# Optimization experiments

Hardware: AMD Instinct MI355X
Metric: run time of the kernel (lower is better)

The kernel has to match this reference:

```python
import jax, jax.numpy as jnp
import numpy as np

V, D, H, F, L, B, S = 32000, 1024, 16, 4096, 6, 2, 1024
DH = D // H


def setup_inputs() -> dict:
    key = jax.random.key(0)
    ks = jax.random.split(key, 12)
    n = lambda k, shape: jax.random.normal(k, shape, jnp.float32) * 0.02
    inp = {}
    inp['x'] = jax.random.randint(ks[0], (B, S), 0, V)
    # causal mask: 1 = masked (upper triangle), matches masked_fill(mask==1, -inf)
    inp['mask'] = jnp.triu(jnp.ones((S, S), jnp.int32), k=1)[None, None]
    inp['embed'] = n(ks[1], (V, D))
    inp['wq'] = n(ks[2], (L, D, D)); inp['bq'] = jnp.zeros((L, D), jnp.float32)
    inp['wk'] = n(ks[3], (L, D, D)); inp['bk'] = jnp.zeros((L, D), jnp.float32)
    inp['wv'] = n(ks[4], (L, D, D)); inp['bv'] = jnp.zeros((L, D), jnp.float32)
    inp['wo'] = n(ks[5], (L, D, D)); inp['bo'] = jnp.zeros((L, D), jnp.float32)
    inp['w1'] = n(ks[6], (L, D, F)); inp['b1'] = jnp.zeros((L, F), jnp.float32)
    inp['w2'] = n(ks[7], (L, F, D)); inp['b2'] = jnp.zeros((L, D), jnp.float32)
    inp['ln1_g'] = jnp.ones((L, D), jnp.float32); inp['ln1_b'] = jnp.zeros((L, D), jnp.float32)
    inp['ln2_g'] = jnp.ones((L, D), jnp.float32); inp['ln2_b'] = jnp.zeros((L, D), jnp.float32)
    inp['lnf_g'] = jnp.ones((D,), jnp.float32); inp['lnf_b'] = jnp.zeros((D,), jnp.float32)
    inp['proj_w'] = n(ks[8], (D, V)); inp['proj_b'] = jnp.zeros((V,), jnp.float32)
    return inp


def _layernorm(x, g, b, eps=1e-5):
    mu = jnp.mean(x, axis=-1, keepdims=True)
    var = jnp.var(x, axis=-1, keepdims=True)
    return (x - mu) * jax.lax.rsqrt(var + eps) * g + b


def _positional_encoding(s, d):
    pos = jnp.arange(s, dtype=jnp.float32)[:, None]
    div = jnp.exp(jnp.arange(0, d, 2, dtype=jnp.float32) * (-jnp.log(10000.0) / d))
    pe = jnp.zeros((s, d), jnp.float32)
    pe = pe.at[:, 0::2].set(jnp.sin(pos * div))
    pe = pe.at[:, 1::2].set(jnp.cos(pos * div))
    return pe


def reference(x, mask, embed, wq, bq, wk, bk, wv, bv, wo, bo, w1, b1, w2, b2,
              ln1_g, ln1_b, ln2_g, ln2_b, lnf_g, lnf_b, proj_w, proj_b):
    b_, s_ = x.shape
    h = embed[x] * jnp.sqrt(jnp.float32(D))          # [B,S,D]
    h = h + _positional_encoding(s_, D)[None]
    scale = 1.0 / jnp.sqrt(jnp.float32(DH))

    def layer(h, p):
        Wq, Bq, Wk, Bk, Wv, Bv, Wo, Bo, W1, B1, W2, B2, G1, Be1, G2, Be2 = p
        q = (h @ Wq + Bq).reshape(b_, s_, H, DH).transpose(0, 2, 1, 3)   # [B,H,S,Dh]
        k = (h @ Wk + Bk).reshape(b_, s_, H, DH).transpose(0, 2, 1, 3)
        v = (h @ Wv + Bv).reshape(b_, s_, H, DH).transpose(0, 2, 1, 3)
        scores = jnp.einsum('bhqd,bhkd->bhqk', q, k) * scale            # [B,H,S,S]
        scores = jnp.where(mask == 1, -jnp.inf, scores)
        attn = jax.nn.softmax(scores, axis=-1)
        ctx = jnp.einsum('bhqk,bhkd->bhqd', attn, v)
        ctx = ctx.transpose(0, 2, 1, 3).reshape(b_, s_, D) @ Wo + Bo
        h = _layernorm(h + ctx, G1, Be1)
        ffn = jax.nn.relu(h @ W1 + B1) @ W2 + B2
        h = _layernorm(h + ffn, G2, Be2)
        return h, None

    h, _ = jax.lax.scan(layer, h, (wq, bq, wk, bk, wv, bv, wo, bo,
                                   w1, b1, w2, b2, ln1_g, ln1_b, ln2_g, ln2_b))
    h = _layernorm(h, lnf_g, lnf_b)
    return h @ proj_w + proj_b                                           # [B,S,V]
```

## Files before the change

### kernel.cpp

```cpp
#include <hip/hip_runtime.h>
#include <math.h>

#define D_MODEL 1024
#define NHEADS 16
#define DHEAD 64
#define FDIM 4096
#define NLAYERS 6
#define BATCH 2
#define SEQ 1024
#define NROWS (BATCH*SEQ)
#define VOCAB 32000

typedef __attribute__((ext_vector_type(4))) float f32x4;
typedef __attribute__((ext_vector_type(4))) __bf16 bf16x4;
typedef __attribute__((ext_vector_type(8))) __bf16 bf16x8;

__device__ __forceinline__ void gll16(const void* g, void* l) {
  __builtin_amdgcn_global_load_lds(
      (const __attribute__((address_space(1))) unsigned int*)g,
      (__attribute__((address_space(3))) unsigned int*)l, 16, 0, 0);
}

__global__ __launch_bounds__(256) void transpose_w(
    const float* __restrict__ W, __bf16* __restrict__ Wt, int K, int N,
    size_t out_lstride, int row_off) {
  __shared__ __bf16 Ls[64][68];
  const float* Wl = W + (size_t)blockIdx.z * K * N;
  __bf16* Wtl = Wt + (size_t)blockIdx.z * out_lstride + (size_t)row_off * K;
  const int n0 = blockIdx.x * 64, k0 = blockIdx.y * 64;
  const int tid = threadIdx.x;
  #pragma unroll
  for (int p = 0; p < 4; ++p) {
    int e = tid + p * 256;
    int r = e >> 4, c4 = (e & 15) * 4;
    float4 v = *(const float4*)&Wl[(size_t)(k0 + r) * N + n0 + c4];
    Ls[c4 + 0][r] = (__bf16)v.x; Ls[c4 + 1][r] = (__bf16)v.y;
    Ls[c4 + 2][r] = (__bf16)v.z; Ls[c4 + 3][r] = (__bf16)v.w;
  }
  __syncthreads();
  #pragma unroll
  for (int p = 0; p < 4; ++p) {
    int e = tid + p * 256;
    int r2 = e >> 4, c8 = (e & 15) * 4;
    bf16x4 o{Ls[r2][c8], Ls[r2][c8 + 1], Ls[r2][c8 + 2], Ls[r2][c8 + 3]};
    *(bf16x4*)&Wtl[(size_t)(n0 + r2) * K + k0 + c8] = o;
  }
}

struct GemmP {
  const __bf16* A;
  const __bf16* W[3];
  const float* B[3];
  void* C[3];
  int N, K;
};

template<int BM, int RELU, int OUTF32, int MULTIBIAS>
__global__ __launch_bounds__(256) void gemm_bf16(GemmP g) {
  constexpr int BK = 64;
  const __bf16* __restrict__ A = g.A;
  const __bf16* __restrict__ W = g.W[blockIdx.z];
  const int N = g.N, K = g.K;

  __shared__ __bf16 As[2][BM * BK];
  __shared__ __bf16 Bs[2][128 * BK];

  const int tid = threadIdx.x;
  const int lane = tid & 63, w = tid >> 6;

  const int gx = gridDim.x;
  const int nblk = gx * gridDim.y;
  const int id = blockIdx.x + blockIdx.y * gx;
  const int per = nblk >> 3;
  const int sid = (id & 7) * per + (id >> 3);
  const int row0 = (sid % gx) * BM;
  const int col0 = (sid / gx) * 128;

  const int wm = w >> 1, wn = w & 1;
  const int lr = lane & 15, rsw = lr & 7;

  constexpr int MI = BM / 32;
  f32x4 acc[MI][4] = {};

  const int swg = ((lane & 7) ^ (lane >> 3)) * 8;
  const __bf16* Ag = A + (size_t)(row0 + w * (BM / 4) + (lane >> 3)) * K + swg;
  const __bf16* Wg = W + (size_t)(col0 + w * 32 + (lane >> 3)) * K + swg;

  const int NT = K / BK;

  auto stage = [&](int buf, int t) {
    const int k0 = t * BK;
    #pragma unroll
    for (int s = 0; s < BM / 32; ++s)
      gll16(Ag + (size_t)s * 8 * K + k0, &As[buf][(w * (BM / 4) + s * 8) * BK]);
    #pragma unroll
    for (int s = 0; s < 4; ++s)
      gll16(Wg + (size_t)s * 8 * K + k0, &Bs[buf][(w * 32 + s * 8) * BK]);
  };

  stage(0, 0);
  __syncthreads();

  int cur = 0;
  for (int t = 0; t < NT; ++t) {
    if (t + 1 < NT) stage(cur ^ 1, t + 1);
    #pragma unroll
    for (int kk = 0; kk < 2; ++kk) {
      const int gsw = ((kk * 4 + (lane >> 4)) ^ rsw) * 8;
      bf16x8 af[MI], bf[4];
      #pragma unroll
      for (int i = 0; i < MI; ++i)
        af[i] = *(const bf16x8*)&As[cur][(wm * (BM / 2) + i * 16 + lr) * BK + gsw];
      #pragma unroll
      for (int j = 0; j < 4; ++j)
        bf[j] = *(const bf16x8*)&Bs[cur][(wn * 64 + j * 16 + lr) * BK + gsw];
      #pragma unroll
      for (int i = 0; i < MI; ++i)
        #pragma unroll
        for (int j = 0; j < 4; ++j)
          acc[i][j] = __builtin_amdgcn_mfma_f32_16x16x32_bf16(af[i], bf[j], acc[i][j], 0, 0, 0);
    }
    __syncthreads();
    cur ^= 1;
  }

  #pragma unroll
  for (int i = 0; i < MI; ++i) {
    #pragma unroll
    for (int j = 0; j < 4; ++j) {
      int col = col0 + wn * 64 + j * 16 + lr;
      float bb = MULTIBIAS ? g.B[col >> 10][col & 1023] : g.B[blockIdx.z][col];
      #pragma unroll
      for (int r = 0; r < 4; ++r) {
        int row = row0 + wm * (BM / 2) + i * 16 + (lane >> 4) * 4 + r;
        float v = acc[i][j][r] + bb;
        if (RELU) v = fmaxf(v, 0.0f);
        if (OUTF32) ((float*)g.C[blockIdx.z])[(size_t)row * N + col] = v;
        else ((__bf16*)g.C[blockIdx.z])[(size_t)row * N + col] = (__bf16)v;
      }
    }
  }
}

__global__ __launch_bounds__(512, 2) void gemm_256(
    const __bf16* __restrict__ A, const __bf16* __restrict__ W,
    const float* __restrict__ bias, float* __restrict__ C, int N, int K) {
  extern __shared__ __bf16 sm[];
  __bf16* Asm = sm;
  __bf16* Bsm = sm + 2 * 256 * 64;

  const int tid = threadIdx.x;
  const int lane = tid & 63, w = tid >> 6;

  const int gx = gridDim.x;
  const int nblk = gx * gridDim.y;
  const int id = blockIdx.x + blockIdx.y * gx;
  const int per = nblk >> 3;
  const int sid = (id & 7) * per + (id >> 3);
  const int row0 = (sid % gx) * 256;
  const int col0 = (sid / gx) * 256;

  const int wr = w >> 2, wc = w & 3;
  const int lr = lane & 15;

  f32x4 acc[8][4] = {};

  const int swg = ((lane & 7) ^ (lane >> 3)) * 8;
  const __bf16* Agb = A + (size_t)(row0 + (lane >> 3)) * K + swg;
  const __bf16* Wgb = W + (size_t)(col0 + (lane >> 3)) * K + swg;

  const int NT = K / 64;

  auto stage_half = [&](int idx) {
    const int tile = idx >> 2, half = idx & 3;
    const int buf = tile & 1;
    const int k0 = tile * 64;
    const int rowbase = (half & 1) * 128 + w * 16;
    const __bf16* src = (half < 2 ? Wgb : Agb) + (size_t)rowbase * K + k0;
    __bf16* dst = (half < 2 ? Bsm : Asm) + buf * 16384 + rowbase * 64;
    gll16(src, dst);
    gll16(src + (size_t)8 * K, dst + 8 * 64);
  };

  #pragma unroll
  for (int i = 0; i < 5; ++i) stage_half(i);
  asm volatile("s_waitcnt vmcnt(2)" ::: "memory");
  __builtin_amdgcn_s_barrier();

  for (int t = 0; t < NT; ++t) {
    const int cur = t & 1;
    bf16x8 bfr[4][2];
    #pragma unroll
    for (int h = 0; h < 4; ++h) {
      if (h == 0) {
        #pragma unroll
        for (int j = 0; j < 4; ++j) {
          int row = wc * 64 + j * 16 + lr;
          #pragma unroll
          for (int kk = 0; kk < 2; ++kk)
            bfr[j][kk] = *(const bf16x8*)&Bsm[cur * 16384 + row * 64 +
                                              (((kk * 4 + (lane >> 4)) ^ (row & 7)) * 8)];
        }
      }
      bf16x8 afr[2][2];
      #pragma unroll
      for (int ii = 0; ii < 2; ++ii) {
        int row = wr * 128 + (2 * h + ii) * 16 + lr;
        #pragma unroll
        for (int kk = 0; kk < 2; ++kk)
          afr[ii][kk] = *(const bf16x8*)&Asm[cur * 16384 + row * 64 +
                                             (((kk * 4 + (lane >> 4)) ^ (row & 7)) * 8)];
      }
      const int sidx = 4 * t + h + 5;
      if (sidx < 4 * NT) stage_half(sidx);
      if (h == 3) {
        if (t + 2 < NT) asm volatile("s_waitcnt vmcnt(2)" ::: "memory");
        else if (t + 1 < NT) asm volatile("s_waitcnt vmcnt(0)" ::: "memory");
      }
      __builtin_amdgcn_s_barrier();
      __builtin_amdgcn_s_setprio(1);
      #pragma unroll
      for (int kk = 0; kk < 2; ++kk)
        #pragma unroll
        for (int ii = 0; ii < 2; ++ii)
          #pragma unroll
          for (int j = 0; j < 4; ++j)
            acc[2 * h + ii][j] = __builtin_amdgcn_mfma_f32_16x16x32_bf16(
                afr[ii][kk], bfr[j][kk], acc[2 * h + ii][j], 0, 0, 0);
      __builtin_amdgcn_s_setprio(0);
      __builtin_amdgcn_s_barrier();
    }
  }

  #pragma unroll
  for (int i = 0; i < 8; ++i) {
    #pragma unroll
    for (int j = 0; j < 4; ++j) {
      int col = col0 + wc * 64 + j * 16 + lr;
      float bb = bias[col];
      #pragma unroll
      for (int r = 0; r < 4; ++r) {
        int row = row0 + wr * 128 + i * 16 + (lane >> 4) * 4 + r;
        C[(size_t)row * N + col] = acc[i][j][r] + bb;
      }
    }
  }
}

__global__ __launch_bounds__(512) void attn_kernel(
    const __bf16* __restrict__ QKV, __bf16* __restrict__ O) {
  __shared__ __bf16 Ks[64 * 64];
  __shared__ __bf16 Vts[64 * 64];
  __shared__ __bf16 Psm[8][16 * 64];

  const int tid = threadIdx.x;
  const int lane = tid & 63, w = tid >> 6;
  const int q0 = blockIdx.x * 128;
  const int bh = blockIdx.y;
  const int b = bh >> 4, h = bh & 15;
  const size_t qb = ((size_t)b * SEQ) * 3072 + (size_t)h * DHEAD;
  const size_t ob = ((size_t)b * SEQ) * D_MODEL + (size_t)h * DHEAD;

  const int lr = lane & 15;
  const int lk = (lane >> 4) * 8;

  bf16x8 qa[2];
  {
    const __bf16* qp = QKV + qb + (size_t)(q0 + w * 16 + lr) * 3072;
    qa[0] = *(const bf16x8*)&qp[lk];
    qa[1] = *(const bf16x8*)&qp[32 + lk];
  }

  f32x4 o_acc[4] = {};
  float m[4], l[4];
  #pragma unroll
  for (int r = 0; r < 4; ++r) { m[r] = -1e30f; l[r] = 0.0f; }

  const int nck = q0 / 64 + 2;

  for (int ck = 0; ck < nck; ++ck) {
    const int kv0 = ck * 64;
    __syncthreads();
    {
      int r = tid >> 3, d8 = (tid & 7) * 8;
      const size_t grow = qb + (size_t)(kv0 + r) * 3072 + d8;
      bf16x8 kv = *(const bf16x8*)&QKV[grow + 1024];
      *(bf16x8*)&Ks[(r * 64 + d8) ^ ((r & 7) << 3)] = kv;
      bf16x8 vv = *(const bf16x8*)&QKV[grow + 2048];
      #pragma unroll
      for (int j = 0; j < 8; ++j)
        Vts[((d8 + j) * 64 + r) ^ (((d8 + j) & 7) << 3)] = vv[j];
    }
    __syncthreads();

    f32x4 s_acc[4] = {};
    #pragma unroll
    for (int t = 0; t < 4; ++t) {
      int row = t * 16 + lr;
      #pragma unroll
      for (int hh = 0; hh < 2; ++hh) {
        bf16x8 kb = *(const bf16x8*)&Ks[(row * 64 + hh * 32 + lk) ^ ((row & 7) << 3)];
        s_acc[t] = __builtin_amdgcn_mfma_f32_16x16x32_bf16(qa[hh], kb, s_acc[t], 0, 0, 0);
      }
    }

    #pragma unroll
    for (int t = 0; t < 4; ++t) {
      int kvg = kv0 + t * 16 + lr;
      #pragma unroll
      for (int r = 0; r < 4; ++r) {
        float sv = s_acc[t][r] * 0.125f;
        int qg = q0 + w * 16 + (lane >> 4) * 4 + r;
        if (kvg > qg) sv = -1e30f;
        s_acc[t][r] = sv;
      }
    }

    #pragma unroll
    for (int r = 0; r < 4; ++r) {
      float cm = fmaxf(fmaxf(s_acc[0][r], s_acc[1][r]), fmaxf(s_acc[2][r], s_acc[3][r]));
      #pragma unroll
      for (int off = 1; off < 16; off <<= 1) cm = fmaxf(cm, __shfl_xor(cm, off, 64));
      float newm = fmaxf(m[r], cm);
      float sc = __expf(m[r] - newm);
      m[r] = newm;
      float psum = 0.0f;
      #pragma unroll
      for (int t = 0; t < 4; ++t) {
        float p = __expf(s_acc[t][r] - newm);
        s_acc[t][r] = p;
        psum += p;
      }
      #pragma unroll
      for (int off = 1; off < 16; off <<= 1) psum += __shfl_xor(psum, off, 64);
      l[r] = l[r] * sc + psum;
      #pragma unroll
      for (int t = 0; t < 4; ++t) o_acc[t][r] *= sc;
    }

    #pragma unroll
    for (int t = 0; t < 4; ++t) {
      #pragma unroll
      for (int r = 0; r < 4; ++r) {
        int ql = (lane >> 4) * 4 + r;
        Psm[w][(ql * 64 + t * 16 + lr) ^ ((ql & 7) << 3)] = (__bf16)(s_acc[t][r]);
      }
    }

    bf16x8 pa[2];
    #pragma unroll
    for (int hh = 0; hh < 2; ++hh)
      pa[hh] = *(const bf16x8*)&Psm[w][(lr * 64 + hh * 32 + lk) ^ ((lr & 7) << 3)];
    #pragma unroll
    for (int t = 0; t < 4; ++t) {
      int row = t * 16 + lr;
      #pragma unroll
      for (int hh = 0; hh < 2; ++hh) {
        bf16x8 vb = *(const bf16x8*)&Vts[(row * 64 + hh * 32 + lk) ^ ((row & 7) << 3)];
        o_acc[t] = __builtin_amdgcn_mfma_f32_16x16x32_bf16(pa[hh], vb, o_acc[t], 0, 0, 0);
      }
    }
  }

  #pragma unroll
  for (int r = 0; r < 4; ++r) {
    float inv = 1.0f / l[r];
    int qg = q0 + w * 16 + (lane >> 4) * 4 + r;
    #pragma unroll
    for (int t = 0; t < 4; ++t)
      O[ob + (size_t)qg * D_MODEL + t * 16 + lr] = (__bf16)(o_acc[t][r] * inv);
  }
}

template<int HASRES>
__global__ __launch_bounds__(256) void addln_kernel(
    const __bf16* __restrict__ X, const __bf16* __restrict__ Rr,
    const float* __restrict__ g, const float* __restrict__ bb,
    __bf16* __restrict__ Out) {
  const int row = blockIdx.x;
  const int tid = threadIdx.x;
  const size_t rb = (size_t)row * D_MODEL + tid * 4;
  bf16x4 xv = *(const bf16x4*)&X[rb];
  float v[4];
  float s = 0.0f, ss = 0.0f;
  if (HASRES) {
    bf16x4 rv = *(const bf16x4*)&Rr[rb];
    #pragma unroll
    for (int i = 0; i < 4; ++i) {
      v[i] = (float)xv[i] + (float)rv[i];
      s += v[i]; ss += v[i] * v[i];
    }
  } else {
    #pragma unroll
    for (int i = 0; i < 4; ++i) { v[i] = (float)xv[i]; s += v[i]; ss += v[i] * v[i]; }
  }
  #pragma unroll
  for (int off = 32; off; off >>= 1) { s += __shfl_xor(s, off, 64); ss += __shfl_xor(ss, off, 64); }
  __shared__ float red[8];
  const int lane = tid & 63, w = tid >> 6;
  if (lane == 0) { red[w] = s; red[4 + w] = ss; }
  __syncthreads();
  s = red[0] + red[1] + red[2] + red[3];
  ss = red[4] + red[5] + red[6] + red[7];
  float mean = s * (1.0f / D_MODEL);
  float var = ss * (1.0f / D_MODEL) - mean * mean;
  float rs = rsqrtf(var + 1e-5f);
  const int d0 = tid * 4;
  bf16x4 ov;
  #pragma unroll
  for (int i = 0; i < 4; ++i)
    ov[i] = (__bf16)((v[i] - mean) * rs * g[d0 + i] + bb[d0 + i]);
  *(bf16x4*)&Out[rb] = ov;
}

__global__ __launch_bounds__(256) void embed_kernel(
    const int* __restrict__ x, const float* __restrict__ embed,
    __bf16* __restrict__ H) {
  const int row = blockIdx.x;
  const int spos = row & (SEQ - 1);
  const int tok = x[row];
  const int tid = threadIdx.x;
  const int d0 = tid * 4;
  float4 e4 = *(const float4*)&embed[(size_t)tok * D_MODEL + d0];
  float ev[4] = {e4.x, e4.y, e4.z, e4.w};
  bf16x4 ov;
  #pragma unroll
  for (int i = 0; i < 4; ++i) {
    int d = d0 + i;
    float div = expf((float)(2 * (d >> 1)) * (-9.2103403719761836f / (float)D_MODEL));
    float ang = (float)spos * div;
    float pe = (d & 1) ? cosf(ang) : sinf(ang);
    ov[i] = (__bf16)(ev[i] * 32.0f + pe);
  }
  *(bf16x4*)&H[(size_t)row * D_MODEL + d0] = ov;
}

extern "C" void kernel_launch(void* const* d_in, const int* in_sizes, int n_in,
                              void* d_out, int out_size, void* d_ws, size_t ws_size,
                              hipStream_t stream) {
  const int* x = (const int*)d_in[0];
  const float* embed = (const float*)d_in[2];
  const float* wq = (const float*)d_in[3];
  const float* bq = (const float*)d_in[4];
  const float* wk = (const float*)d_in[5];
  const float* bk = (const float*)d_in[6];
  const float* wv = (const float*)d_in[7];
  const float* bv = (const float*)d_in[8];
  const float* wo = (const float*)d_in[9];
  const float* bo = (const float*)d_in[10];
  const float* w1 = (const float*)d_in[11];
  const float* b1 = (const float*)d_in[12];
  const float* w2 = (const float*)d_in[13];
  const float* b2 = (const float*)d_in[14];
  const float* ln1g = (const float*)d_in[15];
  const float* ln1b = (const float*)d_in[16];
  const float* ln2g = (const float*)d_in[17];
  const float* ln2b = (const float*)d_in[18];
  const float* lnfg = (const float*)d_in[19];
  const float* lnfb = (const float*)d_in[20];
  const float* pw = (const float*)d_in[21];
  const float* pb = (const float*)d_in[22];
  float* out = (float*)d_out;

  char* wsp = (char*)d_ws;
  size_t off = 0;
  auto alloc = [&](size_t bytes) {
    void* p = wsp + off; off = (off + bytes + 255) & ~(size_t)255; return p;
  };
  const size_t RD2 = (size_t)NROWS * D_MODEL * 2;
  __bf16* Xb   = (__bf16*)alloc(RD2);
  __bf16* QKVb = (__bf16*)alloc((size_t)NROWS * 3072 * 2);
  __bf16* CTXb = (__bf16*)alloc(RD2);
  __bf16* Tb   = (__bf16*)alloc(RD2);
  __bf16* H1b  = (__bf16*)alloc(RD2);
  __bf16* FFb  = QKVb;
  const size_t DD = (size_t)D_MODEL * D_MODEL;
  const size_t DF = (size_t)D_MODEL * FDIM;
  const size_t D3 = (size_t)3072 * D_MODEL;
  __bf16* wqkvt = (__bf16*)alloc(NLAYERS * D3 * 2);
  __bf16* wot = (__bf16*)alloc(NLAYERS * DD * 2);
  __bf16* w1t = (__bf16*)alloc(NLAYERS * DF * 2);
  __bf16* w2t = (__bf16*)alloc(NLAYERS * DF * 2);
  __bf16* pwt = (__bf16*)alloc((size_t)D_MODEL * VOCAB * 2);

  transpose_w<<<dim3(16, 16, NLAYERS), 256, 0, stream>>>(wq, wqkvt, D_MODEL, D_MODEL, D3, 0);
  transpose_w<<<dim3(16, 16, NLAYERS), 256, 0, stream>>>(wk, wqkvt, D_MODEL, D_MODEL, D3, 1024);
  transpose_w<<<dim3(16, 16, NLAYERS), 256, 0, stream>>>(wv, wqkvt, D_MODEL, D_MODEL, D3, 2048);
  transpose_w<<<dim3(16, 16, NLAYERS), 256, 0, stream>>>(wo, wot, D_MODEL, D_MODEL, DD, 0);
  transpose_w<<<dim3(64, 16, NLAYERS), 256, 0, stream>>>(w1, w1t, D_MODEL, FDIM, DF, 0);
  transpose_w<<<dim3(16, 64, NLAYERS), 256, 0, stream>>>(w2, w2t, FDIM, D_MODEL, DF, 0);
  transpose_w<<<dim3(500, 16, 1), 256, 0, stream>>>(pw, pwt, D_MODEL, VOCAB, (size_t)D_MODEL * VOCAB, 0);

  embed_kernel<<<NROWS, 256, 0, stream>>>(x, embed, Xb);

  for (int l = 0; l < NLAYERS; ++l) {
    GemmP g{};
    g.A = Xb; g.N = 3072; g.K = D_MODEL;
    g.W[0] = wqkvt + l * D3;
    g.B[0] = bq + l * D_MODEL; g.B[1] = bk + l * D_MODEL; g.B[2] = bv + l * D_MODEL;
    g.C[0] = QKVb;
    gemm_bf16<64, 0, 0, 1><<<dim3(NROWS / 64, 3072 / 128, 1), 256, 0, stream>>>(g);

    attn_kernel<<<dim3(SEQ / 128, BATCH * NHEADS), 512, 0, stream>>>(QKVb, CTXb);

    GemmP go{};
    go.A = CTXb; go.N = D_MODEL; go.K = D_MODEL;
    go.W[0] = wot + l * DD; go.B[0] = bo + l * D_MODEL; go.C[0] = Tb;
    gemm_bf16<64, 0, 0, 0><<<dim3(NROWS / 64, D_MODEL / 128, 1), 256, 0, stream>>>(go);

    addln_kernel<1><<<NROWS, 256, 0, stream>>>(Xb, Tb, ln1g + l * D_MODEL, ln1b + l * D_MODEL, H1b);

    GemmP g1{};
    g1.A = H1b; g1.N = FDIM; g1.K = D_MODEL;
    g1.W[0] = w1t + l * DF; g1.B[0] = b1 + l * FDIM; g1.C[0] = FFb;
    gemm_bf16<128, 1, 0, 0><<<dim3(NROWS / 128, FDIM / 128, 1), 256, 0, stream>>>(g1);

    GemmP g2{};
    g2.A = FFb; g2.N = D_MODEL; g2.K = FDIM;
    g2.W[0] = w2t + l * DF; g2.B[0] = b2 + l * D_MODEL; g2.C[0] = Tb;
    gemm_bf16<64, 0, 0, 0><<<dim3(NROWS / 64, D_MODEL / 128, 1), 256, 0, stream>>>(g2);

    addln_kernel<1><<<NROWS, 256, 0, stream>>>(H1b, Tb, ln2g + l * D_MODEL, ln2b + l * D_MODEL, Xb);
  }

  addln_kernel<0><<<NROWS, 256, 0, stream>>>(Xb, nullptr, lnfg, lnfb, H1b);

  hipFuncSetAttribute((const void*)gemm_256,
                      hipFuncAttributeMaxDynamicSharedMemorySize, 131072);
  gemm_256<<<dim3(NROWS / 256, VOCAB / 256), 512, 131072, stream>>>(
      H1b, pwt, pb, out, VOCAB, D_MODEL);
}
```

Measured before the change: 1.520 ms.

## Fuse residual add into GEMM epilogue, simplify vocab GEMM pipeline, retile FFN1

The residual add moves into the epilogue of the out-projection and FFN2 GEMMs, and the layernorm kernel drops its residual input. This saves one bf16 read per layernorm, though the residual is now rounded to bf16 together with the GEMM output before normalisation. The vocab-projection GEMM's fine-grained quarter-tile staging, with explicit waitcnt and setprio, is replaced by a plain double-buffered loop with __syncthreads and launch bounds of one block per CU. The FFN1 GEMM switches from BM=128 to BM=64 tiles, which doubles its grid.

```diff
diff --git a/kernel.cpp b/kernel.cpp
--- a/kernel.cpp
+++ b/kernel.cpp
@@ -52,10 +52,11 @@
   const __bf16* W[3];
   const float* B[3];
   void* C[3];
+  const __bf16* Res;
   int N, K;
 };
 
-template<int BM, int RELU, int OUTF32, int MULTIBIAS>
+template<int BM, int RELU, int OUTF32, int MULTIBIAS, int RESADD>
 __global__ __launch_bounds__(256) void gemm_bf16(GemmP g) {
   constexpr int BK = 64;
   const __bf16* __restrict__ A = g.A;
@@ -134,6 +135,7 @@
       for (int r = 0; r < 4; ++r) {
         int row = row0 + wm * (BM / 2) + i * 16 + (lane >> 4) * 4 + r;
         float v = acc[i][j][r] + bb;
+        if (RESADD) v += (float)g.Res[(size_t)row * N + col];
         if (RELU) v = fmaxf(v, 0.0f);
         if (OUTF32) ((float*)g.C[blockIdx.z])[(size_t)row * N + col] = v;
         else ((__bf16*)g.C[blockIdx.z])[(size_t)row * N + col] = (__bf16)v;
@@ -142,12 +144,12 @@
   }
 }
 
-__global__ __launch_bounds__(512, 2) void gemm_256(
+__global__ __launch_bounds__(512, 1) void gemm_256(
     const __bf16* __restrict__ A, const __bf16* __restrict__ W,
     const float* __restrict__ bias, float* __restrict__ C, int N, int K) {
   extern __shared__ __bf16 sm[];
-  __bf16* Asm = sm;
-  __bf16* Bsm = sm + 2 * 256 * 64;
+  __bf16* As = sm;
+  __bf16* Bs = sm + 2 * 256 * 64;
 
   const int tid = threadIdx.x;
   const int lane = tid & 63, w = tid >> 6;
@@ -166,70 +168,49 @@
   f32x4 acc[8][4] = {};
 
   const int swg = ((lane & 7) ^ (lane >> 3)) * 8;
-  const __bf16* Agb = A + (size_t)(row0 + (lane >> 3)) * K + swg;
-  const __bf16* Wgb = W + (size_t)(col0 + (lane >> 3)) * K + swg;
+  const __bf16* Ag = A + (size_t)(row0 + w * 32 + (lane >> 3)) * K + swg;
+  const __bf16* Wg = W + (size_t)(col0 + w * 32 + (lane >> 3)) * K + swg;
 
   const int NT = K / 64;
 
-  auto stage_half = [&](int idx) {
-    const int tile = idx >> 2, half = idx & 3;
-    const int buf = tile & 1;
-    const int k0 = tile * 64;
-    const int rowbase = (half & 1) * 128 + w * 16;
-    const __bf16* src = (half < 2 ? Wgb : Agb) + (size_t)rowbase * K + k0;
-    __bf16* dst = (half < 2 ? Bsm : Asm) + buf * 16384 + rowbase * 64;
-    gll16(src, dst);
-    gll16(src + (size_t)8 * K, dst + 8 * 64);
+  auto stage = [&](int buf, int t) {
+    const int k0 = t * 64;
+    #pragma unroll
+    for (int s = 0; s < 4; ++s) {
+      gll16(Ag + (size_t)(s * 8) * K + k0, &As[buf * 16384 + (w * 32 + s * 8) * 64]);
+      gll16(Wg + (size_t)(s * 8) * K + k0, &Bs[buf * 16384 + (w * 32 + s * 8) * 64]);
+    }
   };
 
-  #pragma unroll
-  for (int i = 0; i < 5; ++i) stage_half(i);
-  asm volatile("s_waitcnt vmcnt(2)" ::: "memory");
-  __builtin_amdgcn_s_barrier();
-
+  stage(0, 0);
+  __syncthreads();
+
+  int cur = 0;
   for (int t = 0; t < NT; ++t) {
-    const int cur = t & 1;
-    bf16x8 bfr[4][2];
-    #pragma unroll
-    for (int h = 0; h < 4; ++h) {
-      if (h == 0) {
+    if (t + 1 < NT) stage(cur ^ 1, t + 1);
+    #pragma unroll
+    for (int kk = 0; kk < 2; ++kk) {
+      bf16x8 af[8], bf[4];
+      #pragma unroll
+      for (int i = 0; i < 8; ++i) {
+        int row = wr * 128 + i * 16 + lr;
+        af[i] = *(const bf16x8*)&As[cur * 16384 + row * 64 +
+                                    (((kk * 4 + (lane >> 4)) ^ (row & 7)) * 8)];
+      }
+      #pragma unroll
+      for (int j = 0; j < 4; ++j) {
+        int row = wc * 64 + j * 16 + lr;
+        bf[j] = *(const bf16x8*)&Bs[cur * 16384 + row * 64 +
+                                    (((kk * 4 + (lane >> 4)) ^ (row & 7)) * 8)];
+      }
+      #pragma unroll
+      for (int i = 0; i < 8; ++i)
         #pragma unroll
-        for (int j = 0; j < 4; ++j) {
-          int row = wc * 64 + j * 16 + lr;
-          #pragma unroll
-          for (int kk = 0; kk < 2; ++kk)
-            bfr[j][kk] = *(const bf16x8*)&Bsm[cur * 16384 + row * 64 +
-                                              (((kk * 4 + (lane >> 4)) ^ (row & 7)) * 8)];
-        }
-      }
-      bf16x8 afr[2][2];
-      #pragma unroll
-      for (int ii = 0; ii < 2; ++ii) {
-        int row = wr * 128 + (2 * h + ii) * 16 + lr;
-        #pragma unroll
-        for (int kk = 0; kk < 2; ++kk)
-          afr[ii][kk] = *(const bf16x8*)&Asm[cur * 16384 + row * 64 +
-                                             (((kk * 4 + (lane >> 4)) ^ (row & 7)) * 8)];
-      }
-      const int sidx = 4 * t + h + 5;
-      if (sidx < 4 * NT) stage_half(sidx);
-      if (h == 3) {
-        if (t + 2 < NT) asm volatile("s_waitcnt vmcnt(2)" ::: "memory");
-        else if (t + 1 < NT) asm volatile("s_waitcnt vmcnt(0)" ::: "memory");
-      }
-      __builtin_amdgcn_s_barrier();
-      __builtin_amdgcn_s_setprio(1);
-      #pragma unroll
-      for (int kk = 0; kk < 2; ++kk)
-        #pragma unroll
-        for (int ii = 0; ii < 2; ++ii)
-          #pragma unroll
-          for (int j = 0; j < 4; ++j)
-            acc[2 * h + ii][j] = __builtin_amdgcn_mfma_f32_16x16x32_bf16(
-                afr[ii][kk], bfr[j][kk], acc[2 * h + ii][j], 0, 0, 0);
-      __builtin_amdgcn_s_setprio(0);
-      __builtin_amdgcn_s_barrier();
-    }
+        for (int j = 0; j < 4; ++j)
+          acc[i][j] = __builtin_amdgcn_mfma_f32_16x16x32_bf16(af[i], bf[j], acc[i][j], 0, 0, 0);
+    }
+    __syncthreads();
+    cur ^= 1;
   }
 
   #pragma unroll
@@ -372,28 +353,17 @@
   }
 }
 
-template<int HASRES>
-__global__ __launch_bounds__(256) void addln_kernel(
-    const __bf16* __restrict__ X, const __bf16* __restrict__ Rr,
-    const float* __restrict__ g, const float* __restrict__ bb,
-    __bf16* __restrict__ Out) {
+__global__ __launch_bounds__(256) void ln_kernel(
+    const __bf16* __restrict__ X, const float* __restrict__ g,
+    const float* __restrict__ bb, __bf16* __restrict__ Out) {
   const int row = blockIdx.x;
   const int tid = threadIdx.x;
   const size_t rb = (size_t)row * D_MODEL + tid * 4;
   bf16x4 xv = *(const bf16x4*)&X[rb];
   float v[4];
   float s = 0.0f, ss = 0.0f;
-  if (HASRES) {
-    bf16x4 rv = *(const bf16x4*)&Rr[rb];
-    #pragma unroll
-    for (int i = 0; i < 4; ++i) {
-      v[i] = (float)xv[i] + (float)rv[i];
-      s += v[i]; ss += v[i] * v[i];
-    }
-  } else {
-    #pragma unroll
-    for (int i = 0; i < 4; ++i) { v[i] = (float)xv[i]; s += v[i]; ss += v[i] * v[i]; }
-  }
+  #pragma unroll
+  for (int i = 0; i < 4; ++i) { v[i] = (float)xv[i]; s += v[i]; ss += v[i] * v[i]; }
   #pragma unroll
   for (int off = 32; off; off >>= 1) { s += __shfl_xor(s, off, 64); ss += __shfl_xor(ss, off, 64); }
   __shared__ float red[8];
@@ -499,31 +469,31 @@
     g.W[0] = wqkvt + l * D3;
     g.B[0] = bq + l * D_MODEL; g.B[1] = bk + l * D_MODEL; g.B[2] = bv + l * D_MODEL;
     g.C[0] = QKVb;
-    gemm_bf16<64, 0, 0, 1><<<dim3(NROWS / 64, 3072 / 128, 1), 256, 0, stream>>>(g);
+    gemm_bf16<64, 0, 0, 1, 0><<<dim3(NROWS / 64, 3072 / 128, 1), 256, 0, stream>>>(g);
 
     attn_kernel<<<dim3(SEQ / 128, BATCH * NHEADS), 512, 0, stream>>>(QKVb, CTXb);
 
     GemmP go{};
     go.A = CTXb; go.N = D_MODEL; go.K = D_MODEL;
-    go.W[0] = wot + l * DD; go.B[0] = bo + l * D_MODEL; go.C[0] = Tb;
-    gemm_bf16<64, 0, 0, 0><<<dim3(NROWS / 64, D_MODEL / 128, 1), 256, 0, stream>>>(go);
-
-    addln_kernel<1><<<NROWS, 256, 0, stream>>>(Xb, Tb, ln1g + l * D_MODEL, ln1b + l * D_MODEL, H1b);
+    go.W[0] = wot + l * DD; go.B[0] = bo + l * D_MODEL; go.C[0] = Tb; go.Res = Xb;
+    gemm_bf16<64, 0, 0, 0, 1><<<dim3(NROWS / 64, D_MODEL / 128, 1), 256, 0, stream>>>(go);
+
+    ln_kernel<<<NROWS, 256, 0, stream>>>(Tb, ln1g + l * D_MODEL, ln1b + l * D_MODEL, H1b);
 
     GemmP g1{};
     g1.A = H1b; g1.N = FDIM; g1.K = D_MODEL;
     g1.W[0] = w1t + l * DF; g1.B[0] = b1 + l * FDIM; g1.C[0] = FFb;
-    gemm_bf16<128, 1, 0, 0><<<dim3(NROWS / 128, FDIM / 128, 1), 256, 0, stream>>>(g1);
+    gemm_bf16<64, 1, 0, 0, 0><<<dim3(NROWS / 64, FDIM / 128, 1), 256, 0, stream>>>(g1);
 
     GemmP g2{};
     g2.A = FFb; g2.N = D_MODEL; g2.K = FDIM;
-    g2.W[0] = w2t + l * DF; g2.B[0] = b2 + l * D_MODEL; g2.C[0] = Tb;
-    gemm_bf16<64, 0, 0, 0><<<dim3(NROWS / 64, D_MODEL / 128, 1), 256, 0, stream>>>(g2);
-
-    addln_kernel<1><<<NROWS, 256, 0, stream>>>(H1b, Tb, ln2g + l * D_MODEL, ln2b + l * D_MODEL, Xb);
-  }
-
-  addln_kernel<0><<<NROWS, 256, 0, stream>>>(Xb, nullptr, lnfg, lnfb, H1b);
+    g2.W[0] = w2t + l * DF; g2.B[0] = b2 + l * D_MODEL; g2.C[0] = Tb; g2.Res = H1b;
+    gemm_bf16<64, 0, 0, 0, 1><<<dim3(NROWS / 64, D_MODEL / 128, 1), 256, 0, stream>>>(g2);
+
+    ln_kernel<<<NROWS, 256, 0, stream>>>(Tb, ln2g + l * D_MODEL, ln2b + l * D_MODEL, Xb);
+  }
+
+  ln_kernel<<<NROWS, 256, 0, stream>>>(Xb, lnfg, lnfb, H1b);
 
   hipFuncSetAttribute((const void*)gemm_256,
                       hipFuncAttributeMaxDynamicSharedMemorySize, 131072);
```

Measured after the change: 1.664 ms. 1.09x slower.
